# Kernel optimization log

Hardware: AMD Instinct MI355X
Metric: run time of the kernel (lower is better)

## Reference

```python
import jax, jax.numpy as jnp
import numpy as np

BATCH, SEQ, IN, HID, CLS = 512, 1024, 64, 256, 10

def setup_inputs() -> dict:
    key = jax.random.key(0)
    k1, k2, k3, k4, k5 = jax.random.split(key, 5)
    s_ih = 1.0 / np.sqrt(IN + HID)
    s_ho = 1.0 / np.sqrt(HID)
    return {
        "inputs": jax.random.normal(k1, (BATCH, SEQ, IN), dtype=jnp.float32),
        "W_ih": jax.random.normal(k2, (IN + HID, HID), dtype=jnp.float32) * s_ih,
        "b_ih": jax.random.normal(k3, (HID,), dtype=jnp.float32) * s_ih,
        "W_ho": jax.random.normal(k4, (HID, CLS), dtype=jnp.float32) * s_ho,
        "b_ho": jax.random.normal(k5, (CLS,), dtype=jnp.float32) * s_ho,
    }

def reference(inputs, W_ih, b_ih, W_ho, b_ho):
    # Elman RNN: hidden_{t} = tanh([x_t, hidden_{t-1}] @ W_ih + b_ih)
    B, S, I = inputs.shape
    H = W_ih.shape[1]
    # split W_ih into input and hidden blocks (equivalent to concat+matmul)
    Wx = W_ih[:I]      # (I, H)
    Wh = W_ih[I:]      # (H, H)
    h0 = jnp.zeros((B, H), dtype=inputs.dtype)
    # precompute input projections for all timesteps at once: (B, S, H)
    xproj = jnp.einsum('bsi,ih->bsh', inputs, Wx) + b_ih

    def step(h, xp_t):
        h_new = jnp.tanh(xp_t + h @ Wh)
        return h_new, None

    h_final, _ = jax.lax.scan(step, h0, jnp.swapaxes(xproj, 0, 1))  # scan over time
    return h_final @ W_ho + b_ho  # (B, CLS)
```

## Files before the change

### kernel.cpp

```cpp
#include <hip/hip_runtime.h>
#include <hip/hip_bf16.h>


#define BATCH 512
#define SEQ   1024
#define INP   64
#define HID   256
#define CLS   10
#define NTHREADS 512
#define TSCALE 2.8853900817779268f

typedef short bf16x8 __attribute__((ext_vector_type(8)));
typedef float f32x4  __attribute__((ext_vector_type(4)));

static __device__ __forceinline__ unsigned short f2bf(float f) {
  __hip_bfloat16 h = __float2bfloat16(f);
  return *reinterpret_cast<unsigned short*>(&h);
}
static __device__ __forceinline__ float bf2f(unsigned short b) {
  union { unsigned int u; float f; } v; v.u = ((unsigned int)b) << 16;
  return v.f;
}
static __device__ __forceinline__ unsigned int cvt_pk_bf16(float lo, float hi) {
  unsigned int r;
  asm("v_cvt_pk_bf16_f32 %0, %1, %2" : "=v"(r) : "v"(lo), "v"(hi));
  return r;
}
static __device__ __forceinline__ float fast_exp2(float x) {
#if __has_builtin(__builtin_amdgcn_exp2f)
  return __builtin_amdgcn_exp2f(x);
#else
  return __exp2f(x);
#endif
}
static __device__ __forceinline__ float fast_rcp(float x) {
#if __has_builtin(__builtin_amdgcn_rcpf)
  return __builtin_amdgcn_rcpf(x);
#else
  return 1.0f / x;
#endif
}
static __device__ __forceinline__ float tanh_scaled(float s) {
  return 1.0f - 2.0f * fast_rcp(1.0f + fast_exp2(s));
}

#define MFMA16(A, B, C) __builtin_amdgcn_mfma_f32_16x16x32_bf16(A, B, C, 0, 0, 0)

#define BARRIER() asm volatile("s_waitcnt lgkmcnt(0)\n\ts_barrier" ::: "memory")

#define STEP(T, CUR, XR) do {                                                   \
     \
     \
    if (lane < 8) {                                                             \
      ((unsigned int*)sX[(CUR) ^ 1])[((scp >> 4) * 2 + srow) * 16 + (scp & 15)] \
          = cvt_pk_bf16(XR.x, XR.y);                                            \
      int tn_ = (T) + 3; tn_ = tn_ < SEQ ? tn_ : SEQ - 1;                       \
      XR = *(const float2*)&xstage[(size_t)tn_ * INP];                          \
    }                                                                           \
    f32x4 acc0a = {bias0, bias0, 0.f, 0.f};                                     \
    f32x4 acc1a = {bias1, bias1, 0.f, 0.f};                                     \
    f32x4 acc0b = {0.f, 0.f, 0.f, 0.f};                                         \
    f32x4 acc1b = {0.f, 0.f, 0.f, 0.f};                                         \
        \
    if (frow < 2) {                                                             \
      fA = *(const bf16x8*)&sX[CUR][0][frow][g8];                               \
      fB = *(const bf16x8*)&sX[CUR][1][frow][g8];                               \
      fC = *(const bf16x8*)&sH[CUR][0][frow][g8];                               \
      fD = *(const bf16x8*)&sH[CUR][1][frow][g8];                               \
      fE = *(const bf16x8*)&sH[CUR][2][frow][g8];                               \
      fF = *(const bf16x8*)&sH[CUR][3][frow][g8];                               \
    }                                                                           \
    acc0a = MFMA16(fA, bw[0][0], acc0a); acc1a = MFMA16(fA, bw[0][1], acc1a);   \
    acc0b = MFMA16(fB, bw[1][0], acc0b); acc1b = MFMA16(fB, bw[1][1], acc1b);   \
    if (frow < 2) {                                                             \
      fA = *(const bf16x8*)&sH[CUR][4][frow][g8];                               \
      fB = *(const bf16x8*)&sH[CUR][5][frow][g8];                               \
    }                                                                           \
    acc0a = MFMA16(fC, bw[2][0], acc0a); acc1a = MFMA16(fC, bw[2][1], acc1a);   \
    acc0b = MFMA16(fD, bw[3][0], acc0b); acc1b = MFMA16(fD, bw[3][1], acc1b);   \
    if (frow < 2) {                                                             \
      fC = *(const bf16x8*)&sH[CUR][6][frow][g8];                               \
      fD = *(const bf16x8*)&sH[CUR][7][frow][g8];                               \
    }                                                                           \
    acc0a = MFMA16(fE, bw[4][0], acc0a); acc1a = MFMA16(fE, bw[4][1], acc1a);   \
    acc0b = MFMA16(fF, bw[5][0], acc0b); acc1b = MFMA16(fF, bw[5][1], acc1b);   \
    acc0a = MFMA16(fA, bw[6][0], acc0a); acc1a = MFMA16(fA, bw[6][1], acc1a);   \
    acc0b = MFMA16(fB, bw[7][0], acc0b); acc1b = MFMA16(fB, bw[7][1], acc1b);   \
    acc0a = MFMA16(fC, bw[8][0], acc0a); acc1a = MFMA16(fC, bw[8][1], acc1a);   \
    acc0b = MFMA16(fD, bw[9][0], acc0b); acc1b = MFMA16(fD, bw[9][1], acc1b);   \
            \
    float t00 = tanh_scaled(acc0a[0] + acc0b[0]);       \
    float t10 = tanh_scaled(acc1a[0] + acc1b[0]);       \
    float t01 = tanh_scaled(acc0a[1] + acc0b[1]);       \
    float t11 = tanh_scaled(acc1a[1] + acc1b[1]);       \
    if (g == 0) {                                                               \
      unsigned int* hd_ = (unsigned int*)sH[(CUR) ^ 1];                         \
      hd_[wave * 32 + frow]      = cvt_pk_bf16(t00, t10);            \
      hd_[wave * 32 + 16 + frow] = cvt_pk_bf16(t01, t11);            \
    }                                                                           \
    BARRIER();                                                                  \
  } while (0)

__global__ __launch_bounds__(NTHREADS, 2)
void rnn_scan_kernel(const float* __restrict__ x,
                     const float* __restrict__ W_ih,
                     const float* __restrict__ b_ih,
                     const float* __restrict__ W_ho,
                     const float* __restrict__ b_ho,
                     float* __restrict__ out) {
  __shared__ __align__(16) unsigned short sH[2][8][2][32];
  __shared__ __align__(16) unsigned short sX[2][2][2][32];

  const int tid  = threadIdx.x;
  const int lane = tid & 63;
  const int wave = tid >> 6;
  const int b0   = blockIdx.x * 2;

  const int g    = (lane >> 4) & 3;
  const int g8   = g * 8;
  const int frow = lane & 15;

  bf16x8 bw[10][2];
  const int colE = 32 * wave + 2 * frow;
  const float bias0 = b_ih[colE] * TSCALE;
  const float bias1 = b_ih[colE + 1] * TSCALE;
#pragma unroll
  for (int q = 0; q < 2; ++q) {
#pragma unroll
    for (int kt = 0; kt < 10; ++kt) {
      bf16x8 v;
#pragma unroll
      for (int i = 0; i < 8; ++i)
        v[i] = (short)f2bf(W_ih[(size_t)(kt * 32 + g * 8 + i) * HID + colE + q] * TSCALE);
      bw[kt][q] = v;
    }
  }

  const int slot = wave * 8 + (lane & 7);
  const int srow = slot >> 5, scp = slot & 31;
  const float* xstage = x + (size_t)(b0 + srow) * SEQ * INP + scp * 2;
  float2 xrA = make_float2(0.f, 0.f), xrB = make_float2(0.f, 0.f);

  bf16x8 fA = {}, fB = {}, fC = {}, fD = {}, fE = {}, fF = {};

  if (tid < 256) ((unsigned int*)sH[0])[tid] = 0u;
  if (lane < 8) {
    float2 v0 = *(const float2*)&xstage[0];
    ((unsigned int*)sX[0])[((scp >> 4) * 2 + srow) * 16 + (scp & 15)]
        = cvt_pk_bf16(v0.x, v0.y);
    xrA = *(const float2*)&xstage[(size_t)1 * INP];
    xrB = *(const float2*)&xstage[(size_t)2 * INP];
  }
  BARRIER();

#pragma unroll 1
  for (int t = 0; t < SEQ; t += 2) {
    STEP(t,     0, xrA);
    STEP(t + 1, 1, xrB);
  }

  if (tid < 2 * CLS) {
    const int r = tid / CLS, cl = tid - r * CLS;
    float s = b_ho[cl];
#pragma unroll 8
    for (int k = 0; k < HID; ++k)
      s += bf2f(sH[0][k >> 5][r][k & 31]) * W_ho[(size_t)k * CLS + cl];
    out[(size_t)(b0 + r) * CLS + cl] = s;
  }
}

extern "C" void kernel_launch(void* const* d_in, const int* in_sizes, int n_in,
                              void* d_out, int out_size, void* d_ws, size_t ws_size,
                              hipStream_t stream) {
  const float* x    = (const float*)d_in[0];
  const float* W_ih = (const float*)d_in[1];
  const float* b_ih = (const float*)d_in[2];
  const float* W_ho = (const float*)d_in[3];
  const float* b_ho = (const float*)d_in[4];
  float* out = (float*)d_out;

  rnn_scan_kernel<<<BATCH / 2, NTHREADS, 0, stream>>>(x, W_ih, b_ih, W_ho, b_ho, out);
}
```

Measured before the change: 537.7 us.

## Pre-accumulate next step's input and own-slice hidden MFMAs before the barrier

Restructures the recurrent step so each wave first consumes the other waves' hidden slices from the previous step (7 k-tiles), computes tanh, then immediately starts the next step's accumulators using the x projection and its own freshly produced hidden slice, before the barrier. This moves 3 of the 10 MFMA k-tiles off the critical post-barrier path, shortening the serial dependency chain per timestep. It requires reordering weight tiles per wave, double-buffered accumulators, preloading two x timesteps, and prefetching x one step further ahead. It also raises register pressure and relies on each wave reading its own just-written slice without a barrier.

Result: slower. 619.3 us (+15.2%).

```diff
diff --git a/kernel.cpp b/kernel.cpp
--- a/kernel.cpp
+++ b/kernel.cpp
@@ -48,55 +48,54 @@
 
 #define BARRIER() asm volatile("s_waitcnt lgkmcnt(0)\n\ts_barrier" ::: "memory")
 
-#define STEP(T, CUR, XR) do {                                                   \
-     \
-     \
-    if (lane < 8) {                                                             \
-      ((unsigned int*)sX[(CUR) ^ 1])[((scp >> 4) * 2 + srow) * 16 + (scp & 15)] \
-          = cvt_pk_bf16(XR.x, XR.y);                                            \
-      int tn_ = (T) + 3; tn_ = tn_ < SEQ ? tn_ : SEQ - 1;                       \
-      XR = *(const float2*)&xstage[(size_t)tn_ * INP];                          \
+#define STEP(T, CUR, AI0a, AI0b, AI1a, AI1b, AO0a, AO0b, AO1a, AO1b, XR) do {   \
+    const int NXT_ = (CUR) ^ 1;                                                 \
+    bf16x8 f0 = {}, f1 = {}, f2 = {}, f3 = {}, f4 = {}, f5 = {}, f6 = {};       \
+    bf16x8 xf0 = {}, xf1 = {};                                                  \
+    if (frow < 2) {                    \
+      f0 = *(const bf16x8*)&sH[CUR][(wave + 1) & 7][frow][g8];                  \
+      f1 = *(const bf16x8*)&sH[CUR][(wave + 2) & 7][frow][g8];                  \
+      f2 = *(const bf16x8*)&sH[CUR][(wave + 3) & 7][frow][g8];                  \
+      f3 = *(const bf16x8*)&sH[CUR][(wave + 4) & 7][frow][g8];                  \
+      f4 = *(const bf16x8*)&sH[CUR][(wave + 5) & 7][frow][g8];                  \
+      f5 = *(const bf16x8*)&sH[CUR][(wave + 6) & 7][frow][g8];                  \
+      f6 = *(const bf16x8*)&sH[CUR][(wave + 7) & 7][frow][g8];                  \
+      xf0 = *(const bf16x8*)&sX[NXT_][0][frow][g8];                             \
+      xf1 = *(const bf16x8*)&sX[NXT_][1][frow][g8];                             \
     }                                                                           \
-    f32x4 acc0a = {bias0, bias0, 0.f, 0.f};                                     \
-    f32x4 acc1a = {bias1, bias1, 0.f, 0.f};                                     \
-    f32x4 acc0b = {0.f, 0.f, 0.f, 0.f};                                         \
-    f32x4 acc1b = {0.f, 0.f, 0.f, 0.f};                                         \
-        \
-    if (frow < 2) {                                                             \
-      fA = *(const bf16x8*)&sX[CUR][0][frow][g8];                               \
-      fB = *(const bf16x8*)&sX[CUR][1][frow][g8];                               \
-      fC = *(const bf16x8*)&sH[CUR][0][frow][g8];                               \
-      fD = *(const bf16x8*)&sH[CUR][1][frow][g8];                               \
-      fE = *(const bf16x8*)&sH[CUR][2][frow][g8];                               \
-      fF = *(const bf16x8*)&sH[CUR][3][frow][g8];                               \
-    }                                                                           \
-    acc0a = MFMA16(fA, bw[0][0], acc0a); acc1a = MFMA16(fA, bw[0][1], acc1a);   \
-    acc0b = MFMA16(fB, bw[1][0], acc0b); acc1b = MFMA16(fB, bw[1][1], acc1b);   \
-    if (frow < 2) {                                                             \
-      fA = *(const bf16x8*)&sH[CUR][4][frow][g8];                               \
-      fB = *(const bf16x8*)&sH[CUR][5][frow][g8];                               \
-    }                                                                           \
-    acc0a = MFMA16(fC, bw[2][0], acc0a); acc1a = MFMA16(fC, bw[2][1], acc1a);   \
-    acc0b = MFMA16(fD, bw[3][0], acc0b); acc1b = MFMA16(fD, bw[3][1], acc1b);   \
-    if (frow < 2) {                                                             \
-      fC = *(const bf16x8*)&sH[CUR][6][frow][g8];                               \
-      fD = *(const bf16x8*)&sH[CUR][7][frow][g8];                               \
-    }                                                                           \
-    acc0a = MFMA16(fE, bw[4][0], acc0a); acc1a = MFMA16(fE, bw[4][1], acc1a);   \
-    acc0b = MFMA16(fF, bw[5][0], acc0b); acc1b = MFMA16(fF, bw[5][1], acc1b);   \
-    acc0a = MFMA16(fA, bw[6][0], acc0a); acc1a = MFMA16(fA, bw[6][1], acc1a);   \
-    acc0b = MFMA16(fB, bw[7][0], acc0b); acc1b = MFMA16(fB, bw[7][1], acc1b);   \
-    acc0a = MFMA16(fC, bw[8][0], acc0a); acc1a = MFMA16(fC, bw[8][1], acc1a);   \
-    acc0b = MFMA16(fD, bw[9][0], acc0b); acc1b = MFMA16(fD, bw[9][1], acc1b);   \
+    AI0a = MFMA16(f0, bwS[0][0], AI0a); AI1a = MFMA16(f0, bwS[0][1], AI1a);     \
+    AI0b = MFMA16(f1, bwS[1][0], AI0b); AI1b = MFMA16(f1, bwS[1][1], AI1b);     \
+    AI0a = MFMA16(f2, bwS[2][0], AI0a); AI1a = MFMA16(f2, bwS[2][1], AI1a);     \
+    AI0b = MFMA16(f3, bwS[3][0], AI0b); AI1b = MFMA16(f3, bwS[3][1], AI1b);     \
+    AI0a = MFMA16(f4, bwS[4][0], AI0a); AI1a = MFMA16(f4, bwS[4][1], AI1a);     \
+    AI0b = MFMA16(f5, bwS[5][0], AI0b); AI1b = MFMA16(f5, bwS[5][1], AI1b);     \
+    AI0a = MFMA16(f6, bwS[6][0], AI0a); AI1a = MFMA16(f6, bwS[6][1], AI1a);     \
             \
-    float t00 = tanh_scaled(acc0a[0] + acc0b[0]);       \
-    float t10 = tanh_scaled(acc1a[0] + acc1b[0]);       \
-    float t01 = tanh_scaled(acc0a[1] + acc0b[1]);       \
-    float t11 = tanh_scaled(acc1a[1] + acc1b[1]);       \
+    float t00 = tanh_scaled(AI0a[0] + AI0b[0]);         \
+    float t10 = tanh_scaled(AI1a[0] + AI1b[0]);         \
+    float t01 = tanh_scaled(AI0a[1] + AI0b[1]);         \
+    float t11 = tanh_scaled(AI1a[1] + AI1b[1]);         \
     if (g == 0) {                                                               \
-      unsigned int* hd_ = (unsigned int*)sH[(CUR) ^ 1];                         \
+      unsigned int* hd_ = (unsigned int*)sH[NXT_];                              \
       hd_[wave * 32 + frow]      = cvt_pk_bf16(t00, t10);            \
       hd_[wave * 32 + 16 + frow] = cvt_pk_bf16(t01, t11);            \
+    }                                                                           \
+                              \
+    AO0a = f32x4{bias0, bias0, 0.f, 0.f};                                       \
+    AO1a = f32x4{bias1, bias1, 0.f, 0.f};                                       \
+    AO0b = f32x4{0.f, 0.f, 0.f, 0.f};                                           \
+    AO1b = f32x4{0.f, 0.f, 0.f, 0.f};                                           \
+    bf16x8 fown = {};                                                           \
+    if (frow < 2) fown = *(const bf16x8*)&sH[NXT_][wave][frow][g8];             \
+    AO0a = MFMA16(xf0, bwS[8][0], AO0a); AO1a = MFMA16(xf0, bwS[8][1], AO1a);   \
+    AO0b = MFMA16(xf1, bwS[9][0], AO0b); AO1b = MFMA16(xf1, bwS[9][1], AO1b);   \
+    AO0a = MFMA16(fown, bwS[7][0], AO0a); AO1a = MFMA16(fown, bwS[7][1], AO1a); \
+          \
+    if (lane < 8) {                                                             \
+      ((unsigned int*)sX[CUR])[((scp >> 4) * 2 + srow) * 16 + (scp & 15)]       \
+          = cvt_pk_bf16(XR.x, XR.y);                                            \
+      int tn_ = (T) + 4; tn_ = tn_ < SEQ ? tn_ : SEQ - 1;                       \
+      XR = *(const float2*)&xstage[(size_t)tn_ * INP];                          \
     }                                                                           \
     BARRIER();                                                                  \
   } while (0)
@@ -120,43 +119,67 @@
   const int g8   = g * 8;
   const int frow = lane & 15;
 
-  bf16x8 bw[10][2];
+  bf16x8 bwS[10][2];
   const int colE = 32 * wave + 2 * frow;
   const float bias0 = b_ih[colE] * TSCALE;
   const float bias1 = b_ih[colE + 1] * TSCALE;
 #pragma unroll
-  for (int q = 0; q < 2; ++q) {
+  for (int i = 0; i < 10; ++i) {
+    int krow0;
+    if (i < 7)       krow0 = INP + ((wave + 1 + i) & 7) * 32;
+    else if (i == 7) krow0 = INP + wave * 32;
+    else             krow0 = (i - 8) * 32;
 #pragma unroll
-    for (int kt = 0; kt < 10; ++kt) {
+    for (int q = 0; q < 2; ++q) {
       bf16x8 v;
 #pragma unroll
-      for (int i = 0; i < 8; ++i)
-        v[i] = (short)f2bf(W_ih[(size_t)(kt * 32 + g * 8 + i) * HID + colE + q] * TSCALE);
-      bw[kt][q] = v;
+      for (int e = 0; e < 8; ++e)
+        v[e] = (short)f2bf(W_ih[(size_t)(krow0 + g * 8 + e) * HID + colE + q] * TSCALE);
+      bwS[i][q] = v;
     }
   }
 
   const int slot = wave * 8 + (lane & 7);
   const int srow = slot >> 5, scp = slot & 31;
   const float* xstage = x + (size_t)(b0 + srow) * SEQ * INP + scp * 2;
-  float2 xrA = make_float2(0.f, 0.f), xrB = make_float2(0.f, 0.f);
-
-  bf16x8 fA = {}, fB = {}, fC = {}, fD = {}, fE = {}, fF = {};
+  float2 xrE = make_float2(0.f, 0.f), xrO = make_float2(0.f, 0.f);
 
   if (tid < 256) ((unsigned int*)sH[0])[tid] = 0u;
+  if (tid < 128) {
+    const int tt = tid >> 6;
+    const int sl = tid & 63;
+    const int r = sl >> 5, cp = sl & 31;
+    const float2 v = *(const float2*)&x[((size_t)(b0 + r) * SEQ + tt) * INP + cp * 2];
+    ((unsigned int*)sX[tt])[((cp >> 4) * 2 + r) * 16 + (cp & 15)]
+        = cvt_pk_bf16(v.x, v.y);
+  }
   if (lane < 8) {
-    float2 v0 = *(const float2*)&xstage[0];
-    ((unsigned int*)sX[0])[((scp >> 4) * 2 + srow) * 16 + (scp & 15)]
-        = cvt_pk_bf16(v0.x, v0.y);
-    xrA = *(const float2*)&xstage[(size_t)1 * INP];
-    xrB = *(const float2*)&xstage[(size_t)2 * INP];
+    xrE = *(const float2*)&xstage[(size_t)2 * INP];
+    xrO = *(const float2*)&xstage[(size_t)3 * INP];
   }
   BARRIER();
+
+  f32x4 aE0a, aE0b, aE1a, aE1b, aO0a, aO0b, aO1a, aO1b;
+  {
+    bf16x8 xf0 = {}, xf1 = {}, fown = {};
+    if (frow < 2) {
+      xf0 = *(const bf16x8*)&sX[0][0][frow][g8];
+      xf1 = *(const bf16x8*)&sX[0][1][frow][g8];
+      fown = *(const bf16x8*)&sH[0][wave][frow][g8];
+    }
+    aE0a = f32x4{bias0, bias0, 0.f, 0.f};
+    aE1a = f32x4{bias1, bias1, 0.f, 0.f};
+    aE0b = f32x4{0.f, 0.f, 0.f, 0.f};
+    aE1b = f32x4{0.f, 0.f, 0.f, 0.f};
+    aE0a = MFMA16(xf0, bwS[8][0], aE0a); aE1a = MFMA16(xf0, bwS[8][1], aE1a);
+    aE0b = MFMA16(xf1, bwS[9][0], aE0b); aE1b = MFMA16(xf1, bwS[9][1], aE1b);
+    aE0a = MFMA16(fown, bwS[7][0], aE0a); aE1a = MFMA16(fown, bwS[7][1], aE1a);
+  }
 
 #pragma unroll 1
   for (int t = 0; t < SEQ; t += 2) {
-    STEP(t,     0, xrA);
-    STEP(t + 1, 1, xrB);
+    STEP(t,     0, aE0a, aE0b, aE1a, aE1b, aO0a, aO0b, aO1a, aO1b, xrE);
+    STEP(t + 1, 1, aO0a, aO0b, aO1a, aO1b, aE0a, aE0b, aE1a, aE1b, xrO);
   }
 
   if (tid < 2 * CLS) {
```
